# Performance work log

Hardware: AMD Instinct MI355X
Metric: run time of the kernel (lower is better)

## Reference

```python
import jax, jax.numpy as jnp
import numpy as np

D_MODEL = 1024
N_HEADS = 16
HEAD_DIM = D_MODEL // N_HEADS


def setup_inputs() -> dict:
    key = jax.random.key(0)
    k_x, k_wqkv, k_bqkv, k_wo, k_bo = jax.random.split(key, 5)
    B, T = 2, 2048
    scale = 1.0 / np.sqrt(D_MODEL)
    return {
        "x": jax.random.normal(k_x, (B, T, D_MODEL), dtype=jnp.float32),
        "W_qkv": jax.random.normal(k_wqkv, (D_MODEL, 3 * D_MODEL), dtype=jnp.float32) * scale,
        "b_qkv": jax.random.normal(k_bqkv, (3 * D_MODEL,), dtype=jnp.float32) * 0.01,
        "W_out": jax.random.normal(k_wo, (D_MODEL, D_MODEL), dtype=jnp.float32) * scale,
        "b_out": jax.random.normal(k_bo, (D_MODEL,), dtype=jnp.float32) * 0.01,
    }


def reference(x, W_qkv, b_qkv, W_out, b_out):
    B, T, C = x.shape
    qkv = x @ W_qkv + b_qkv                      # [B,T,3C]
    q, k, v = jnp.split(qkv, 3, axis=-1)
    def heads(t):
        return t.reshape(B, T, N_HEADS, HEAD_DIM).transpose(0, 2, 1, 3)  # [B,H,T,d]
    q, k, v = heads(q), heads(k), heads(v)
    att = jnp.einsum('bhqd,bhkd->bhqk', q, k) / np.sqrt(HEAD_DIM)
    causal = jnp.tril(jnp.ones((T, T), dtype=bool))
    att = jnp.where(causal, att, -jnp.inf)
    att = jax.nn.softmax(att, axis=-1)
    out = jnp.einsum('bhqk,bhkd->bhqd', att, v)  # [B,H,T,d]
    out = out.transpose(0, 2, 1, 3).reshape(B, T, C)
    return out @ W_out + b_out
```

## Files before the change

### kernel.cpp

```cpp
#include <hip/hip_runtime.h>
#include <hip/hip_bf16.h>
#include <math.h>

typedef __bf16 bf16;
typedef __attribute__((ext_vector_type(8))) __bf16 bf16x8;
typedef __attribute__((ext_vector_type(4))) __bf16 bf16x4;
typedef __attribute__((ext_vector_type(4))) float f32x4;
typedef __attribute__((ext_vector_type(16))) float f32x16;
typedef __attribute__((ext_vector_type(4))) unsigned u32x4;

#define T_SEQ 2048

static __device__ __forceinline__ float fast_exp2(float x) {
#if __has_builtin(__builtin_amdgcn_exp2f)
    return __builtin_amdgcn_exp2f(x);
#else
    return __expf(x * 0.69314718f);
#endif
}

static __device__ __forceinline__ unsigned pk(float lo, float hi) {
    unsigned a = (unsigned)__builtin_bit_cast(unsigned short, (bf16)lo);
    unsigned b = (unsigned)__builtin_bit_cast(unsigned short, (bf16)hi);
    return a | (b << 16);
}

static __device__ __forceinline__ void gload_lds16(const bf16* g, bf16* l) {
    __builtin_amdgcn_global_load_lds((const __attribute__((address_space(1))) void*)g,
                                     (__attribute__((address_space(3))) void*)l, 16, 0, 0);
}

static __device__ __forceinline__ int swz(int row, int colb) {
    return row * 128 + (colb ^ ((row & 7) << 4));
}

__global__ void convert_kernel(const float* __restrict__ x, bf16* __restrict__ xb, int n4)
{
    int i = blockIdx.x * blockDim.x + threadIdx.x;
    int stride = gridDim.x * blockDim.x;
    for (; i < n4; i += stride) {
        f32x4 v = ((const f32x4*)x)[i];
        bf16x4 o;
        o[0] = (bf16)v[0]; o[1] = (bf16)v[1]; o[2] = (bf16)v[2]; o[3] = (bf16)v[3];
        ((bf16x4*)xb)[i] = o;
    }
}

__global__ __launch_bounds__(256) void transpose_conv_kernel(
    const float* __restrict__ W, bf16* __restrict__ Wt, int K, int N)
{
    __shared__ float tile[32][33];
    int tx = threadIdx.x & 31, ty = threadIdx.x >> 5;
    int n0 = blockIdx.x * 32, k0 = blockIdx.y * 32;
#pragma unroll
    for (int j = 0; j < 4; ++j)
        tile[ty + j * 8][tx] = W[(size_t)(k0 + ty + j * 8) * N + n0 + tx];
    __syncthreads();
#pragma unroll
    for (int j = 0; j < 4; ++j)
        Wt[(size_t)(n0 + ty + j * 8) * K + k0 + tx] = (bf16)tile[tx][ty + j * 8];
}

__global__ __launch_bounds__(256) void vtrans_kernel(
    const bf16* __restrict__ qkv, bf16* __restrict__ Vt)
{
    __shared__ bf16 tile[64][72];
    const int tid = threadIdx.x;
    const int bh = blockIdx.y, b = bh >> 4, h = bh & 15;
    const int t0 = blockIdx.x * 64;
    const size_t base = (size_t)b * T_SEQ * 3072 + 2048 + h * 64;
    const int r = tid >> 3, c = (tid & 7) * 8;
    *(bf16x8*)&tile[r][c]      = *(const bf16x8*)&qkv[base + (size_t)(t0 + r) * 3072 + c];
    *(bf16x8*)&tile[r + 32][c] = *(const bf16x8*)&qkv[base + (size_t)(t0 + r + 32) * 3072 + c];
    __syncthreads();
    bf16x8 o0, o1;
#pragma unroll
    for (int j = 0; j < 8; ++j) { o0[j] = tile[c + j][r]; o1[j] = tile[c + j][r + 32]; }
    *(bf16x8*)&Vt[((size_t)bh * 64 + r) * T_SEQ + t0 + c] = o0;
    *(bf16x8*)&Vt[((size_t)bh * 64 + r + 32) * T_SEQ + t0 + c] = o1;
}

template<int BM, int BN, int BLK, int WGN, int OUT_BF16>
__global__ __launch_bounds__(BLK, 2) void gemm2ph_kernel(
    const bf16* __restrict__ A, const bf16* __restrict__ Bt,
    const float* __restrict__ bias, void* __restrict__ Cout,
    int M, int N, int K, int GX)
{
    constexpr int WAVES = BLK / 64, WGM = WAVES / WGN;
    constexpr int MR = BM / (WGM * 16), NR = BN / (WGN * 16);
    constexpr int A_RND = BM * 8 / BLK, B_RND = BN * 8 / BLK;
    constexpr int LDS_HALF = (BM + BN) * 128;
    __shared__ __align__(16) char lds[2 * LDS_HALF];

    const int tid = threadIdx.x, lane = tid & 63, wid = tid >> 6;
    const int wm = wid / WGN, wn = wid % WGN;
    const int l15 = lane & 15, l4 = lane >> 4;
    const int cpx = gridDim.x >> 3;
    const int sbid = ((int)blockIdx.x & 7) * cpx + ((int)blockIdx.x >> 3);
    const int m0 = (sbid / GX) * BM, n0 = (sbid % GX) * BN;
    const int wu = tid & ~63;

    f32x4 acc[MR][NR] = {};
    const int NT = K >> 6;

    auto stage = [&](int b, int kt) {
        char* Ab = lds + b * LDS_HALF;
        char* Bb = Ab + BM * 128;
#pragma unroll
        for (int j = 0; j < A_RND; ++j) {
            int ch = j * BLK + tid, r = ch >> 3;
            int c = ((ch & 7) ^ (r & 7)) * 8;
            gload_lds16(&A[(size_t)(m0 + r) * K + kt + c],
                        (bf16*)Ab + (size_t)(j * BLK + wu) * 8);
        }
#pragma unroll
        for (int j = 0; j < B_RND; ++j) {
            int ch = j * BLK + tid, r = ch >> 3;
            int c = ((ch & 7) ^ (r & 7)) * 8;
            gload_lds16(&Bt[(size_t)(n0 + r) * K + kt + c],
                        (bf16*)Bb + (size_t)(j * BLK + wu) * 8);
        }
    };

    stage(0, 0);
    asm volatile("s_waitcnt vmcnt(0)" ::: "memory");
    __builtin_amdgcn_s_barrier();

    for (int t = 0; t < NT; ++t) {
        if (t + 1 < NT) stage((t + 1) & 1, (t + 1) * 64);
        const char* Ab = lds + (t & 1) * LDS_HALF;
        const char* Bb = Ab + BM * 128;
#pragma unroll
        for (int kk = 0; kk < 2; ++kk) {
            bf16x8 af[MR], bfr[NR];
#pragma unroll
            for (int mi = 0; mi < MR; ++mi) {
                int row = wm * (MR * 16) + mi * 16 + l15;
                af[mi] = *(const bf16x8*)(Ab + swz(row, kk * 64 + l4 * 16));
            }
#pragma unroll
            for (int ni = 0; ni < NR; ++ni) {
                int row = wn * (NR * 16) + ni * 16 + l15;
                bfr[ni] = *(const bf16x8*)(Bb + swz(row, kk * 64 + l4 * 16));
            }
#pragma unroll
            for (int mi = 0; mi < MR; ++mi)
#pragma unroll
                for (int ni = 0; ni < NR; ++ni)
                    acc[mi][ni] = __builtin_amdgcn_mfma_f32_16x16x32_bf16(
                        af[mi], bfr[ni], acc[mi][ni], 0, 0, 0);
        }
        asm volatile("s_waitcnt vmcnt(0)" ::: "memory");
        __builtin_amdgcn_s_barrier();
    }

#pragma unroll
    for (int mi = 0; mi < MR; ++mi) {
#pragma unroll
        for (int ni = 0; ni < NR; ++ni) {
            int col = n0 + wn * (NR * 16) + ni * 16 + l15;
            float bv = bias[col];
#pragma unroll
            for (int r = 0; r < 4; ++r) {
                int row = m0 + wm * (MR * 16) + mi * 16 + l4 * 4 + r;
                float v = acc[mi][ni][r] + bv;
                if (OUT_BF16) ((bf16*)Cout)[(size_t)row * N + col] = (bf16)v;
                else          ((float*)Cout)[(size_t)row * N + col] = v;
            }
        }
    }
}

__global__ __launch_bounds__(256, 3) void attn_kernel(
    const bf16* __restrict__ qkv, const bf16* __restrict__ Vt, bf16* __restrict__ attb)
{
    __shared__ __align__(16) char smem[32768];
    const int tid = threadIdx.x, lane = tid & 63, wid = tid >> 6;
    const int qg = wid >> 1, par = wid & 1;
    const int bid = blockIdx.x;
    const int iq = 31 - (bid >> 5);
    const int bh = bid & 31, b = bh >> 4, h = bh & 15;
    const int nt = iq + 1, npairs = (nt + 1) >> 1;
    const int l31 = lane & 31, hi = lane >> 5, hib = hi * 16;
    const size_t base = (size_t)b * T_SEQ * 3072;
    const int koff = 1024 + h * 64;
    const size_t vtb = (size_t)bh * 64 * T_SEQ;
    const int sr = tid >> 2, sq4 = tid & 3;

    const int q0 = iq * 64 + qg * 32;
    const int qrow = q0 + l31;

    bf16x8 Qf[4];
#pragma unroll
    for (int ds = 0; ds < 4; ++ds)
        Qf[ds] = *(const bf16x8*)&qkv[base + (size_t)qrow * 3072 + h * 64 + ds * 16 + hi * 8];

    bf16x8 onesA;
#pragma unroll
    for (int j = 0; j < 8; ++j) onesA[j] = (bf16)1.0f;

    f32x16 Oacc[2] = {};
    f32x16 lacc = {};

    bf16x8 kreg[2][2], vreg[2][2];
    {
#pragma unroll
        for (int p = 0; p < 2; ++p)
#pragma unroll
            for (int j = 0; j < 2; ++j) {
                kreg[p][j] = *(const bf16x8*)&qkv[base + (size_t)(p * 64 + sr) * 3072
                                                 + koff + sq4 * 16 + j * 8];
                vreg[p][j] = *(const bf16x8*)&Vt[vtb + (size_t)sr * T_SEQ + p * 64 + sq4 * 16 + j * 8];
            }
    }

    for (int u = 0; u < npairs; ++u) {
        __syncthreads();
#pragma unroll
        for (int p = 0; p < 2; ++p) {
            char* Kp = smem + p * 8192;
            char* Vp = smem + 16384 + p * 8192;
#pragma unroll
            for (int j = 0; j < 2; ++j) {
                const int byte = swz(sr, sq4 * 32 + j * 16);
                *(bf16x8*)(Kp + byte) = kreg[p][j];
                *(bf16x8*)(Vp + byte) = vreg[p][j];
            }
        }
        __syncthreads();
        if (u + 1 < npairs) {
            const int pb = (u + 1) * 128;
#pragma unroll
            for (int p = 0; p < 2; ++p)
#pragma unroll
                for (int j = 0; j < 2; ++j) {
                    kreg[p][j] = *(const bf16x8*)&qkv[base + (size_t)(pb + p * 64 + sr) * 3072
                                                     + koff + sq4 * 16 + j * 8];
                    vreg[p][j] = *(const bf16x8*)&Vt[vtb + (size_t)sr * T_SEQ + pb + p * 64 + sq4 * 16 + j * 8];
                }
        }
        const int t = 2 * u + par;
        if (t < nt) {
            const char* Kc = smem + par * 8192;
            const char* Vc = smem + 16384 + par * 8192;
            f32x16 S[2] = {};
            __builtin_amdgcn_s_setprio(1);
#pragma unroll
            for (int ds = 0; ds < 4; ++ds)
#pragma unroll
                for (int kt = 0; kt < 2; ++kt) {
                    bf16x8 af = *(const bf16x8*)(Kc + swz(kt * 32 + l31, ds * 32 + hib));
                    S[kt] = __builtin_amdgcn_mfma_f32_32x32x16_bf16(af, Qf[ds], S[kt], 0, 0, 0);
                }
            __builtin_amdgcn_s_setprio(0);
            if (t == nt - 1) {
                const int qloc = qg * 32 + l31;
#pragma unroll
                for (int kt = 0; kt < 2; ++kt)
#pragma unroll
                    for (int j = 0; j < 16; ++j) {
                        const int kloc = kt * 32 + (j & 3) + 8 * (j >> 2) + 4 * hi;
                        if (kloc > qloc) S[kt][j] = -3.0e38f;
                    }
            }
#pragma unroll
            for (int kt = 0; kt < 2; ++kt)
#pragma unroll
                for (int j = 0; j < 16; ++j)
                    S[kt][j] = fast_exp2(S[kt][j] * 0.18033688f);
            __builtin_amdgcn_s_setprio(1);
#pragma unroll
            for (int ks = 0; ks < 4; ++ks) {
                const int kt = ks >> 1, bs = (ks & 1) * 8;
                unsigned P01 = pk(S[kt][bs + 0], S[kt][bs + 1]);
                unsigned P23 = pk(S[kt][bs + 2], S[kt][bs + 3]);
                unsigned P45 = pk(S[kt][bs + 4], S[kt][bs + 5]);
                unsigned P67 = pk(S[kt][bs + 6], S[kt][bs + 7]);
                auto r02 = __builtin_amdgcn_permlane32_swap(P01, P45, false, false);
                auto r13 = __builtin_amdgcn_permlane32_swap(P23, P67, false, false);
                u32x4 wv;
                wv[0] = r02[0]; wv[1] = r13[0]; wv[2] = r02[1]; wv[3] = r13[1];
                bf16x8 Bfrag = __builtin_bit_cast(bf16x8, wv);
#pragma unroll
                for (int dt = 0; dt < 2; ++dt) {
                    bf16x8 av = *(const bf16x8*)(Vc + swz(dt * 32 + l31, ks * 32 + hib));
                    Oacc[dt] = __builtin_amdgcn_mfma_f32_32x32x16_bf16(av, Bfrag, Oacc[dt], 0, 0, 0);
                }
                lacc = __builtin_amdgcn_mfma_f32_32x32x16_bf16(onesA, Bfrag, lacc, 0, 0, 0);
            }
            __builtin_amdgcn_s_setprio(0);
        }
    }

    float* cbuf = (float*)smem;
    __syncthreads();
    if (par == 1) {
        float* p = cbuf + (qg * 64 + lane) * 36;
#pragma unroll
        for (int dt = 0; dt < 2; ++dt)
#pragma unroll
            for (int j = 0; j < 16; ++j) p[dt * 16 + j] = Oacc[dt][j];
        p[32] = lacc[0];
    }
    __syncthreads();
    if (par == 0) {
        const float* p = cbuf + (qg * 64 + lane) * 36;
        float inv = 1.f / (lacc[0] + p[32]);
#pragma unroll
        for (int dt = 0; dt < 2; ++dt) {
#pragma unroll
            for (int g = 0; g < 4; ++g) {
                bf16x4 o;
#pragma unroll
                for (int j = 0; j < 4; ++j)
                    o[j] = (bf16)((Oacc[dt][g * 4 + j] + p[dt * 16 + g * 4 + j]) * inv);
                const int d = dt * 32 + g * 8 + 4 * hi;
                *(bf16x4*)&attb[((size_t)b * T_SEQ + qrow) * 1024 + h * 64 + d] = o;
            }
        }
    }
}

extern "C" void kernel_launch(void* const* d_in, const int* in_sizes, int n_in,
                              void* d_out, int out_size, void* d_ws, size_t ws_size,
                              hipStream_t stream)
{
    const float* x    = (const float*)d_in[0];
    const float* Wqkv = (const float*)d_in[1];
    const float* bqkv = (const float*)d_in[2];
    const float* Wout = (const float*)d_in[3];
    const float* bout = (const float*)d_in[4];
    float* out = (float*)d_out;

    char* ws = (char*)d_ws;
    bf16* xb    = (bf16*)(ws);
    bf16* Vt    = (bf16*)(ws);
    bf16* Wqkvt = (bf16*)(ws + (8ull  << 20));
    bf16* Woutt = (bf16*)(ws + (14ull << 20));
    bf16* qkvb  = (bf16*)(ws + (16ull << 20));
    bf16* attb  = (bf16*)(ws + (40ull << 20));

    convert_kernel<<<dim3(2048), dim3(256), 0, stream>>>(x, xb, (4096 * 1024) / 4);
    transpose_conv_kernel<<<dim3(96, 32), dim3(256), 0, stream>>>(Wqkv, Wqkvt, 1024, 3072);
    transpose_conv_kernel<<<dim3(32, 32), dim3(256), 0, stream>>>(Wout, Woutt, 1024, 1024);
    gemm2ph_kernel<128, 192, 256, 2, 1><<<dim3(512), dim3(256), 0, stream>>>(
        xb, Wqkvt, bqkv, (void*)qkvb, 4096, 3072, 1024, 16);
    vtrans_kernel<<<dim3(32, 32), dim3(256), 0, stream>>>(qkvb, Vt);
    attn_kernel<<<dim3(1024), dim3(256), 0, stream>>>(qkvb, Vt, attb);
    gemm2ph_kernel<128, 128, 256, 2, 0><<<dim3(256), dim3(256), 0, stream>>>(
        attb, Woutt, bout, (void*)out, 4096, 1024, 1024, 8);
}
```

Before: 97.06 us.

## Double query tile per attention block to reuse K/V tiles across two query halves

Each attention block now handles 128 query rows instead of 64, and each wave holds two 32-row query fragments that share every K/V fragment loaded from shared memory. The grid shrinks from 1024 to 512 blocks. The row-sum is now computed with VALU adds plus a lane shuffle instead of an extra MFMA against a ones matrix. The goal is to halve global and LDS traffic for K/V per query and drop the extra MFMA. In exchange, register pressure roughly doubles (occupancy bound lowered from 3 to 2), shared memory grows, and causal load balance across blocks becomes coarser.

After: 105.9 us. +9.1%, slower.

```diff
diff --git a/kernel.cpp b/kernel.cpp
--- a/kernel.cpp
+++ b/kernel.cpp
@@ -171,36 +171,34 @@
     }
 }
 
-__global__ __launch_bounds__(256, 3) void attn_kernel(
+__global__ __launch_bounds__(256, 2) void attn_kernel(
     const bf16* __restrict__ qkv, const bf16* __restrict__ Vt, bf16* __restrict__ attb)
 {
-    __shared__ __align__(16) char smem[32768];
+    __shared__ __align__(16) char smem[36864];
     const int tid = threadIdx.x, lane = tid & 63, wid = tid >> 6;
     const int qg = wid >> 1, par = wid & 1;
     const int bid = blockIdx.x;
-    const int iq = 31 - (bid >> 5);
+    const int iq = 15 - (bid >> 5);
     const int bh = bid & 31, b = bh >> 4, h = bh & 15;
-    const int nt = iq + 1, npairs = (nt + 1) >> 1;
+    const int npairs = iq + 1;
     const int l31 = lane & 31, hi = lane >> 5, hib = hi * 16;
     const size_t base = (size_t)b * T_SEQ * 3072;
     const int koff = 1024 + h * 64;
     const size_t vtb = (size_t)bh * 64 * T_SEQ;
     const int sr = tid >> 2, sq4 = tid & 3;
 
-    const int q0 = iq * 64 + qg * 32;
-    const int qrow = q0 + l31;
-
-    bf16x8 Qf[4];
-#pragma unroll
-    for (int ds = 0; ds < 4; ++ds)
-        Qf[ds] = *(const bf16x8*)&qkv[base + (size_t)qrow * 3072 + h * 64 + ds * 16 + hi * 8];
-
-    bf16x8 onesA;
-#pragma unroll
-    for (int j = 0; j < 8; ++j) onesA[j] = (bf16)1.0f;
-
-    f32x16 Oacc[2] = {};
-    f32x16 lacc = {};
+    const int q0 = iq * 128 + qg * 64;
+
+    bf16x8 Qf[2][4];
+#pragma unroll
+    for (int qh = 0; qh < 2; ++qh)
+#pragma unroll
+        for (int ds = 0; ds < 4; ++ds)
+            Qf[qh][ds] = *(const bf16x8*)&qkv[base + (size_t)(q0 + qh * 32 + l31) * 3072
+                                             + h * 64 + ds * 16 + hi * 8];
+
+    f32x16 Oacc[2][2] = {};
+    float l_run[2] = { 0.f, 0.f };
 
     bf16x8 kreg[2][2], vreg[2][2];
     {
@@ -240,53 +238,71 @@
                 }
         }
         const int t = 2 * u + par;
-        if (t < nt) {
-            const char* Kc = smem + par * 8192;
-            const char* Vc = smem + 16384 + par * 8192;
+        const int k0g = t * 64;
+        const char* Kc = smem + par * 8192;
+        const char* Vc = smem + 16384 + par * 8192;
+        const bool domask = (k0g + 63 > q0);
+
+#pragma unroll 1
+        for (int kt = 0; kt < 2; ++kt) {
             f32x16 S[2] = {};
             __builtin_amdgcn_s_setprio(1);
 #pragma unroll
-            for (int ds = 0; ds < 4; ++ds)
-#pragma unroll
-                for (int kt = 0; kt < 2; ++kt) {
-                    bf16x8 af = *(const bf16x8*)(Kc + swz(kt * 32 + l31, ds * 32 + hib));
-                    S[kt] = __builtin_amdgcn_mfma_f32_32x32x16_bf16(af, Qf[ds], S[kt], 0, 0, 0);
-                }
+            for (int ds = 0; ds < 4; ++ds) {
+                bf16x8 af = *(const bf16x8*)(Kc + swz(kt * 32 + l31, ds * 32 + hib));
+#pragma unroll
+                for (int qh = 0; qh < 2; ++qh)
+                    S[qh] = __builtin_amdgcn_mfma_f32_32x32x16_bf16(af, Qf[qh][ds], S[qh], 0, 0, 0);
+            }
             __builtin_amdgcn_s_setprio(0);
-            if (t == nt - 1) {
-                const int qloc = qg * 32 + l31;
-#pragma unroll
-                for (int kt = 0; kt < 2; ++kt)
+            if (domask) {
+#pragma unroll
+                for (int qh = 0; qh < 2; ++qh) {
+                    const int qglob = q0 + qh * 32 + l31;
 #pragma unroll
                     for (int j = 0; j < 16; ++j) {
-                        const int kloc = kt * 32 + (j & 3) + 8 * (j >> 2) + 4 * hi;
-                        if (kloc > qloc) S[kt][j] = -3.0e38f;
+                        const int kglob = k0g + kt * 32 + (j & 3) + 8 * (j >> 2) + 4 * hi;
+                        if (kglob > qglob) S[qh][j] = -3.0e38f;
                     }
-            }
-#pragma unroll
-            for (int kt = 0; kt < 2; ++kt)
-#pragma unroll
-                for (int j = 0; j < 16; ++j)
-                    S[kt][j] = fast_exp2(S[kt][j] * 0.18033688f);
+                }
+            }
+#pragma unroll
+            for (int qh = 0; qh < 2; ++qh) {
+                float ls = 0.f;
+#pragma unroll
+                for (int j = 0; j < 16; ++j) {
+                    float p = fast_exp2(S[qh][j] * 0.18033688f);
+                    S[qh][j] = p;
+                    ls += p;
+                }
+                ls += __shfl_xor(ls, 32);
+                l_run[qh] += ls;
+            }
             __builtin_amdgcn_s_setprio(1);
 #pragma unroll
-            for (int ks = 0; ks < 4; ++ks) {
-                const int kt = ks >> 1, bs = (ks & 1) * 8;
-                unsigned P01 = pk(S[kt][bs + 0], S[kt][bs + 1]);
-                unsigned P23 = pk(S[kt][bs + 2], S[kt][bs + 3]);
-                unsigned P45 = pk(S[kt][bs + 4], S[kt][bs + 5]);
-                unsigned P67 = pk(S[kt][bs + 6], S[kt][bs + 7]);
-                auto r02 = __builtin_amdgcn_permlane32_swap(P01, P45, false, false);
-                auto r13 = __builtin_amdgcn_permlane32_swap(P23, P67, false, false);
-                u32x4 wv;
-                wv[0] = r02[0]; wv[1] = r13[0]; wv[2] = r02[1]; wv[3] = r13[1];
-                bf16x8 Bfrag = __builtin_bit_cast(bf16x8, wv);
+            for (int ks2 = 0; ks2 < 2; ++ks2) {
+                const int ks = kt * 2 + ks2, bs = ks2 * 8;
+                bf16x8 Bfrag[2];
+#pragma unroll
+                for (int qh = 0; qh < 2; ++qh) {
+                    unsigned P01 = pk(S[qh][bs + 0], S[qh][bs + 1]);
+                    unsigned P23 = pk(S[qh][bs + 2], S[qh][bs + 3]);
+                    unsigned P45 = pk(S[qh][bs + 4], S[qh][bs + 5]);
+                    unsigned P67 = pk(S[qh][bs + 6], S[qh][bs + 7]);
+                    auto r02 = __builtin_amdgcn_permlane32_swap(P01, P45, false, false);
+                    auto r13 = __builtin_amdgcn_permlane32_swap(P23, P67, false, false);
+                    u32x4 wv;
+                    wv[0] = r02[0]; wv[1] = r13[0]; wv[2] = r02[1]; wv[3] = r13[1];
+                    Bfrag[qh] = __builtin_bit_cast(bf16x8, wv);
+                }
 #pragma unroll
                 for (int dt = 0; dt < 2; ++dt) {
                     bf16x8 av = *(const bf16x8*)(Vc + swz(dt * 32 + l31, ks * 32 + hib));
-                    Oacc[dt] = __builtin_amdgcn_mfma_f32_32x32x16_bf16(av, Bfrag, Oacc[dt], 0, 0, 0);
-                }
-                lacc = __builtin_amdgcn_mfma_f32_32x32x16_bf16(onesA, Bfrag, lacc, 0, 0, 0);
+#pragma unroll
+                    for (int qh = 0; qh < 2; ++qh)
+                        Oacc[qh][dt] = __builtin_amdgcn_mfma_f32_32x32x16_bf16(
+                            av, Bfrag[qh], Oacc[qh][dt], 0, 0, 0);
+                }
             }
             __builtin_amdgcn_s_setprio(0);
         }
@@ -295,27 +311,33 @@
     float* cbuf = (float*)smem;
     __syncthreads();
     if (par == 1) {
-        float* p = cbuf + (qg * 64 + lane) * 36;
-#pragma unroll
-        for (int dt = 0; dt < 2; ++dt)
-#pragma unroll
-            for (int j = 0; j < 16; ++j) p[dt * 16 + j] = Oacc[dt][j];
-        p[32] = lacc[0];
+        float* p = cbuf + (qg * 64 + lane) * 68;
+#pragma unroll
+        for (int qh = 0; qh < 2; ++qh)
+#pragma unroll
+            for (int dt = 0; dt < 2; ++dt)
+#pragma unroll
+                for (int j = 0; j < 16; ++j) p[qh * 32 + dt * 16 + j] = Oacc[qh][dt][j];
+        p[64] = l_run[0]; p[65] = l_run[1];
     }
     __syncthreads();
     if (par == 0) {
-        const float* p = cbuf + (qg * 64 + lane) * 36;
-        float inv = 1.f / (lacc[0] + p[32]);
-#pragma unroll
-        for (int dt = 0; dt < 2; ++dt) {
-#pragma unroll
-            for (int g = 0; g < 4; ++g) {
-                bf16x4 o;
-#pragma unroll
-                for (int j = 0; j < 4; ++j)
-                    o[j] = (bf16)((Oacc[dt][g * 4 + j] + p[dt * 16 + g * 4 + j]) * inv);
-                const int d = dt * 32 + g * 8 + 4 * hi;
-                *(bf16x4*)&attb[((size_t)b * T_SEQ + qrow) * 1024 + h * 64 + d] = o;
+        const float* p = cbuf + (qg * 64 + lane) * 68;
+#pragma unroll
+        for (int qh = 0; qh < 2; ++qh) {
+            float inv = 1.f / (l_run[qh] + p[64 + qh]);
+            const int qrow = q0 + qh * 32 + l31;
+#pragma unroll
+            for (int dt = 0; dt < 2; ++dt) {
+#pragma unroll
+                for (int g = 0; g < 4; ++g) {
+                    bf16x4 o;
+#pragma unroll
+                    for (int j = 0; j < 4; ++j)
+                        o[j] = (bf16)((Oacc[qh][dt][g * 4 + j] + p[qh * 32 + dt * 16 + g * 4 + j]) * inv);
+                    const int d = dt * 32 + g * 8 + 4 * hi;
+                    *(bf16x4*)&attb[((size_t)b * T_SEQ + qrow) * 1024 + h * 64 + d] = o;
+                }
             }
         }
     }
@@ -346,7 +368,7 @@
     gemm2ph_kernel<128, 192, 256, 2, 1><<<dim3(512), dim3(256), 0, stream>>>(
         xb, Wqkvt, bqkv, (void*)qkvb, 4096, 3072, 1024, 16);
     vtrans_kernel<<<dim3(32, 32), dim3(256), 0, stream>>>(qkvb, Vt);
-    attn_kernel<<<dim3(1024), dim3(256), 0, stream>>>(qkvb, Vt, attb);
+    attn_kernel<<<dim3(512), dim3(256), 0, stream>>>(qkvb, Vt, attb);
     gemm2ph_kernel<128, 128, 256, 2, 0><<<dim3(256), dim3(256), 0, stream>>>(
         attb, Woutt, bout, (void*)out, 4096, 1024, 1024, 8);
 }
```
